# Performance work log

Hardware: AMD Instinct MI355X
Metric: run time of the kernel (lower is better)

The kernel has to match this reference:

```python
import jax, jax.numpy as jnp
import numpy as np

# ---- module hyperparameters (match init_kwargs) ----
SPATIAL = (32, 64)          # token grid, N = 32*64 = 2048
D_MODEL = 1024
N_HEADS = 16
HEAD_DIM = D_MODEL // N_HEADS  # 64
THETA = 10000.0
XPOS_SCALE_BASE = SPATIAL[0] * 2  # 64


def _rope_tables():
    """ND rotary (xpos) tables, lucidrains-style.
    Each spatial axis gets head_dim//ndim rotary channels; frequencies are
    interleave-repeated (r=2) to pair with rotate_half. Returns cos, sin,
    xpos scale, each [N, HEAD_DIM] float32."""
    nd = len(SPATIAL)
    dpa = HEAD_DIM // nd  # dims per axis (32)
    freqs_axes, scale_axes = [], []
    for size in SPATIAL:
        inv_freq = 1.0 / (THETA ** (np.arange(0, dpa, 2, dtype=np.float64) / dpa))
        t = np.arange(size, dtype=np.float64)
        f = np.repeat(t[:, None] * inv_freq[None, :], 2, axis=-1)        # [size, dpa]
        sbase = (np.arange(0, dpa, 2, dtype=np.float64) + 0.4 * dpa) / (1.4 * dpa)
        power = (t - size // 2) / XPOS_SCALE_BASE
        sc = np.repeat(sbase[None, :] ** power[:, None], 2, axis=-1)     # [size, dpa]
        freqs_axes.append(f)
        scale_axes.append(sc)
    # broadcast each axis table over the full grid, concat along channel dim
    def grid_concat(tabs):
        parts = []
        for i, tab in enumerate(tabs):
            shp = [1] * nd + [dpa]
            shp[i] = SPATIAL[i]
            parts.append(np.broadcast_to(tab.reshape(shp), tuple(SPATIAL) + (dpa,)))
        return np.concatenate(parts, axis=-1).reshape(-1, HEAD_DIM)  # [N, HEAD_DIM]
    freqs = grid_concat(freqs_axes)
    xscale = grid_concat(scale_axes)
    return (jnp.asarray(np.cos(freqs), jnp.float32),
            jnp.asarray(np.sin(freqs), jnp.float32),
            jnp.asarray(xscale, jnp.float32))


def _rotate_half(x):
    # pairwise rotation: (x1, x2) -> (-x2, x1), interleaved layout
    x = x.reshape(*x.shape[:-1], -1, 2)
    x1, x2 = x[..., 0], x[..., 1]
    return jnp.stack((-x2, x1), axis=-1).reshape(*x.shape[:-2], -1)


def setup_inputs() -> dict:
    key = jax.random.key(0)
    ks = jax.random.split(key, 3)
    B, N = 2, SPATIAL[0] * SPATIAL[1]
    x = jax.random.normal(ks[0], (B, N, D_MODEL), dtype=jnp.float32)
    w_qkv = jax.random.normal(ks[1], (D_MODEL, 3 * D_MODEL), dtype=jnp.float32) * 0.02
    b_qkv = jnp.zeros((3 * D_MODEL,), jnp.float32)
    w_proj = jax.random.normal(ks[2], (D_MODEL, D_MODEL), dtype=jnp.float32) * 0.02
    b_proj = jnp.zeros((D_MODEL,), jnp.float32)
    return {"x": x, "w_qkv": w_qkv, "b_qkv": b_qkv, "w_proj": w_proj, "b_proj": b_proj}


def reference(x, w_qkv, b_qkv, w_proj, b_proj):
    B, N, C = x.shape
    scale = HEAD_DIM ** -0.5
    qkv = (x @ w_qkv + b_qkv).reshape(B, N, 3, N_HEADS, HEAD_DIM)
    qkv = qkv.transpose(2, 0, 3, 1, 4)  # [3, B, H, N, D]
    q, k, v = qkv[0], qkv[1], qkv[2]
    cos, sin, xs = _rope_tables()       # [N, D], broadcast over B,H
    q = (q * cos + _rotate_half(q) * sin) * xs
    k = (k * cos + _rotate_half(k) * sin) / xs
    attn = jax.nn.softmax(jnp.einsum('bhnd,bhmd->bhnm', q, k) * scale, axis=-1)
    out = jnp.einsum('bhnm,bhmd->bhnd', attn, v)
    out = out.transpose(0, 2, 1, 3).reshape(B, N, C)
    return out @ w_proj + b_proj
```

## Files before the change

### kernel.cpp

```cpp
#include <hip/hip_runtime.h>
#include <math.h>

typedef __attribute__((ext_vector_type(8))) _Float16 f16x8;
typedef __attribute__((ext_vector_type(4))) _Float16 f16x4;
typedef __attribute__((ext_vector_type(4))) float f32x4;
typedef __attribute__((ext_vector_type(16))) float f32x16;

#define MFMAH(a, b, c) __builtin_amdgcn_mfma_f32_16x16x32_f16((a), (b), (c), 0, 0, 0)
#define MFMA32(a, b, c) __builtin_amdgcn_mfma_f32_32x32x16_f16((a), (b), (c), 0, 0, 0)

#define QSCALE 0.18033688011112042f
#define SOFF 4.328085122666891f


__device__ __forceinline__ void gl_lds16(const _Float16* g, _Float16* l) {
    __builtin_amdgcn_global_load_lds(
        (const __attribute__((address_space(1))) unsigned int*)g,
        (__attribute__((address_space(3))) unsigned int*)l, 16, 0, 0);
}

__device__ __forceinline__ unsigned pkh(float a, float b) {
    union { _Float16 h[2]; unsigned u; } x;
    x.h[0] = (_Float16)a;
    x.h[1] = (_Float16)b;
    return x.u;
}

__global__ void prep_kernel(const float* __restrict__ x, const float* __restrict__ w_qkv,
                            const float* __restrict__ w_proj, _Float16* __restrict__ xb,
                            _Float16* __restrict__ wq, _Float16* __restrict__ wp,
                            float* __restrict__ ct, float* __restrict__ st,
                            float* __restrict__ xt) {
    __shared__ float tile[32][33];
    const int b = blockIdx.x, tid = threadIdx.x;
    if (b < 4096) {
        int i = (b * 256 + tid) * 4;
        float4 v = *(const float4*)&x[i];
        f16x4 h = {(_Float16)v.x, (_Float16)v.y, (_Float16)v.z, (_Float16)v.w};
        *(f16x4*)&xb[i] = h;
    } else if (b < 4096 + 3072 + 1024) {
        int t, C;
        const float* src;
        _Float16* dst;
        if (b < 4096 + 3072) { t = b - 4096; C = 3072; src = w_qkv; dst = wq; }
        else                 { t = b - 4096 - 3072; C = 1024; src = w_proj; dst = wp; }
        const int tr = t & 31, tc = t >> 5;
        const int tx = tid & 31, ty = tid >> 5;
#pragma unroll
        for (int yy = 0; yy < 4; ++yy) {
            int r = ty + yy * 8;
            tile[r][tx] = src[(size_t)(tr * 32 + r) * C + tc * 32 + tx];
        }
        __syncthreads();
#pragma unroll
        for (int yy = 0; yy < 4; ++yy) {
            int r = ty + yy * 8;
            dst[(size_t)(tc * 32 + r) * 1024 + tr * 32 + tx] = (_Float16)tile[tx][r];
        }
    } else {
        int i = (b - 8192) * 256 + tid;
        int n = i >> 6, d = i & 63;
        int gi = n >> 6, gj = n & 63;
        int axis = d >> 5;
        int p = (d & 31) >> 1;
        float t = axis ? (float)gj : (float)gi;
        float half = axis ? 32.0f : 16.0f;
        float inv_freq = powf(10000.0f, -(float)p * (1.0f / 16.0f));
        float fr = t * inv_freq;
        float sbase = (2.0f * p + 12.8f) / 44.8f;
        float xs = powf(sbase, (t - half) * (1.0f / 64.0f));
        ct[i] = cosf(fr);
        st[i] = sinf(fr);
        xt[i] = xs;
    }
}

__global__ __launch_bounds__(256) void gemm_qkv_kernel(
    const _Float16* __restrict__ A_g, const _Float16* __restrict__ B_g,
    const float* __restrict__ bias, const float* __restrict__ ctab,
    const float* __restrict__ stab, const float* __restrict__ xtab,
    _Float16* __restrict__ qb, _Float16* __restrict__ kb, _Float16* __restrict__ vt) {
    __shared__ __align__(16) _Float16 Asm[4096];
    __shared__ __align__(16) _Float16 Bsm[4096];

    const int tid = threadIdx.x;
    const int lane = tid & 63, wave = tid >> 6;
    const int quad = lane >> 4, l16 = lane & 15;
    const int wm = wave >> 1, wn = wave & 1;
    const int m0 = blockIdx.x * 128, n0 = blockIdx.y * 128;

    f32x4 zero = {0.f, 0.f, 0.f, 0.f};
    f32x4 acc[4][4];
#pragma unroll
    for (int i = 0; i < 4; ++i)
#pragma unroll
        for (int j = 0; j < 4; ++j) acc[i][j] = zero;

    const int c1t = tid + 256;
    const int row0 = tid >> 2, s0 = tid & 3;
    const int row1 = c1t >> 2, s1 = c1t & 3;
    const int g0 = s0 ^ ((row0 >> 1) & 3);
    const int g1 = s1 ^ ((row1 >> 1) & 3);
    const _Float16* Ap0 = &A_g[(size_t)(m0 + row0) * 1024 + (g0 << 3)];
    const _Float16* Ap1 = &A_g[(size_t)(m0 + row1) * 1024 + (g1 << 3)];
    const _Float16* Bp0 = &B_g[(size_t)(n0 + row0) * 1024 + (g0 << 3)];
    const _Float16* Bp1 = &B_g[(size_t)(n0 + row1) * 1024 + (g1 << 3)];
    _Float16* La0 = &Asm[tid * 8];
    _Float16* La1 = &Asm[c1t * 8];
    _Float16* Lb0 = &Bsm[tid * 8];
    _Float16* Lb1 = &Bsm[c1t * 8];

    const int sw = (l16 >> 1) & 3;

    for (int k0 = 0; k0 < 1024; k0 += 32) {
        __syncthreads();
        gl_lds16(Ap0 + k0, La0);
        gl_lds16(Ap1 + k0, La1);
        gl_lds16(Bp0 + k0, Lb0);
        gl_lds16(Bp1 + k0, Lb1);
        __syncthreads();

        f16x8 af[4], bf[4];
#pragma unroll
        for (int i = 0; i < 4; ++i) {
            af[i] = *(const f16x8*)&Asm[(wm * 64 + i * 16 + l16) * 32 + ((quad ^ sw) << 3)];
            bf[i] = *(const f16x8*)&Bsm[(wn * 64 + i * 16 + l16) * 32 + ((quad ^ sw) << 3)];
        }
#pragma unroll
        for (int i = 0; i < 4; ++i)
#pragma unroll
            for (int j = 0; j < 4; ++j) acc[i][j] = MFMAH(af[i], bf[j], acc[i][j]);
    }

    float bj[4];
#pragma unroll
    for (int j = 0; j < 4; ++j) bj[j] = bias[n0 + wn * 64 + j * 16 + l16];

    if (n0 < 2048) {
#pragma unroll
        for (int i = 0; i < 4; ++i) {
#pragma unroll
            for (int r = 0; r < 4; ++r) {
                const int row = m0 + wm * 64 + i * 16 + quad * 4 + r;
                const int b = row >> 11, nrow = row & 2047;
#pragma unroll
                for (int j = 0; j < 4; ++j) {
                    const int col = n0 + wn * 64 + j * 16 + l16;
                    float v = acc[i][j][r] + bj[j];
                    float partner = __shfl_xor(v, 1);
                    const int hh = (col >> 6) & 15;
                    const int d = col & 63;
                    const size_t o = ((size_t)(b * 16 + hh) * 2048 + nrow) * 64 + d;
                    float rh = (d & 1) ? partner : -partner;
                    const int ti = nrow * 64 + d;
                    float rv = v * ctab[ti] + rh * stab[ti];
                    float xs = xtab[ti];
                    if (col < 1024)
                        qb[o] = (_Float16)(rv * xs * QSCALE);
                    else
                        kb[o] = (_Float16)(rv / xs);
                }
            }
        }
    } else {
#pragma unroll
        for (int i = 0; i < 4; ++i) {
            const int row = m0 + wm * 64 + i * 16 + quad * 4;
            const int b = row >> 11, nrow = row & 2047;
            const int nrp = (nrow & ~12) | ((nrow & 4) << 1) | ((nrow & 8) >> 1);
#pragma unroll
            for (int j = 0; j < 4; ++j) {
                const int col = n0 + wn * 64 + j * 16 + l16;
                const int hh = (col >> 6) & 15;
                const int d = col & 63;
                f16x4 pv4;
#pragma unroll
                for (int r = 0; r < 4; ++r) pv4[r] = (_Float16)(acc[i][j][r] + bj[j]);
                *(f16x4*)&vt[((size_t)(b * 16 + hh) * 64 + d) * 2048 + nrp] = pv4;
            }
        }
    }
}

__global__ __launch_bounds__(256) void gemm_proj_kernel(
    const _Float16* __restrict__ A_g, const _Float16* __restrict__ B_g,
    const float* __restrict__ bias, float* __restrict__ out) {
    __shared__ __align__(16) _Float16 Asm[4096];
    __shared__ __align__(16) _Float16 Bsm[4096];

    const int tid = threadIdx.x;
    const int lane = tid & 63, wave = tid >> 6;
    const int quad = lane >> 4, l16 = lane & 15;
    const int wm = wave >> 1, wn = wave & 1;
    const int m0 = blockIdx.x * 128, n0 = blockIdx.y * 128;

    f32x4 zero = {0.f, 0.f, 0.f, 0.f};
    f32x4 acc[4][4];
#pragma unroll
    for (int i = 0; i < 4; ++i)
#pragma unroll
        for (int j = 0; j < 4; ++j) acc[i][j] = zero;

    const int c1t = tid + 256;
    const int row0 = tid >> 2, s0 = tid & 3;
    const int row1 = c1t >> 2, s1 = c1t & 3;
    const int g0 = s0 ^ ((row0 >> 1) & 3);
    const int g1 = s1 ^ ((row1 >> 1) & 3);
    const _Float16* Ap0 = &A_g[(size_t)(m0 + row0) * 1024 + (g0 << 3)];
    const _Float16* Ap1 = &A_g[(size_t)(m0 + row1) * 1024 + (g1 << 3)];
    const _Float16* Bp0 = &B_g[(size_t)(n0 + row0) * 1024 + (g0 << 3)];
    const _Float16* Bp1 = &B_g[(size_t)(n0 + row1) * 1024 + (g1 << 3)];
    _Float16* La0 = &Asm[tid * 8];
    _Float16* La1 = &Asm[c1t * 8];
    _Float16* Lb0 = &Bsm[tid * 8];
    _Float16* Lb1 = &Bsm[c1t * 8];

    const int sw = (l16 >> 1) & 3;

    for (int k0 = 0; k0 < 1024; k0 += 32) {
        __syncthreads();
        gl_lds16(Ap0 + k0, La0);
        gl_lds16(Ap1 + k0, La1);
        gl_lds16(Bp0 + k0, Lb0);
        gl_lds16(Bp1 + k0, Lb1);
        __syncthreads();

        f16x8 af[4], bf[4];
#pragma unroll
        for (int i = 0; i < 4; ++i) {
            af[i] = *(const f16x8*)&Asm[(wm * 64 + i * 16 + l16) * 32 + ((quad ^ sw) << 3)];
            bf[i] = *(const f16x8*)&Bsm[(wn * 64 + i * 16 + l16) * 32 + ((quad ^ sw) << 3)];
        }
#pragma unroll
        for (int i = 0; i < 4; ++i)
#pragma unroll
            for (int j = 0; j < 4; ++j) acc[i][j] = MFMAH(af[i], bf[j], acc[i][j]);
    }

    float bj[4];
#pragma unroll
    for (int j = 0; j < 4; ++j) bj[j] = bias[n0 + wn * 64 + j * 16 + l16];
#pragma unroll
    for (int i = 0; i < 4; ++i)
#pragma unroll
        for (int r = 0; r < 4; ++r) {
            const int row = m0 + wm * 64 + i * 16 + quad * 4 + r;
#pragma unroll
            for (int j = 0; j < 4; ++j) {
                const int col = n0 + wn * 64 + j * 16 + l16;
                out[(size_t)row * 1024 + col] = acc[i][j][r] + bj[j];
            }
        }
}

#define KLD 72

__global__ __launch_bounds__(512) void attn_kernel(
    const _Float16* __restrict__ qb, const _Float16* __restrict__ kb,
    const _Float16* __restrict__ vt, _Float16* __restrict__ ao) {
    __shared__ __align__(16) _Float16 smem[8 * 64 * KLD];

    const int tid = threadIdx.x;
    const int lane = tid & 63, wave = tid >> 6;
    const int w4 = wave & 3, wgrp = wave >> 2;
    const int l32 = lane & 31, hi = lane >> 5, hi8 = hi << 3;
    const int bh = blockIdx.x & 31, qt = blockIdx.x >> 5;
    const size_t base = (size_t)bh * 2048 * 64;
    const int qrow0 = qt * 128 + w4 * 32;
    const int kbase = wgrp << 10;

    _Float16* K0 = &smem[(wgrp * 2 + 0) * 64 * KLD];
    _Float16* K1 = &smem[(wgrp * 2 + 1) * 64 * KLD];
    _Float16* V0 = &smem[(4 + wgrp * 2 + 0) * 64 * KLD];
    _Float16* V1 = &smem[(4 + wgrp * 2 + 1) * 64 * KLD];

    f16x8 qf[4];
#pragma unroll
    for (int dc = 0; dc < 4; ++dc)
        qf[dc] = *(const f16x8*)&qb[base + (size_t)(qrow0 + l32) * 64 + dc * 16 + hi8];

    f32x16 moff16, zero16;
#pragma unroll
    for (int e = 0; e < 16; ++e) { moff16[e] = -SOFF; zero16[e] = 0.f; }
    f32x16 o0 = zero16, o1 = zero16;
    float lsum = 0.f;

    const int t256 = tid & 255;
    const int kr0 = t256 >> 3, ko0 = (t256 & 7) << 3;
    const int kr1 = kr0 + 32;
    f16x8 pk0, pk1, pv0, pv1;
    auto gload = [&](int kt) {
        pk0 = *(const f16x8*)&kb[base + (size_t)(kt + kr0) * 64 + ko0];
        pk1 = *(const f16x8*)&kb[base + (size_t)(kt + kr1) * 64 + ko0];
        pv0 = *(const f16x8*)&vt[((size_t)bh * 64 + kr0) * 2048 + kt + ko0];
        pv1 = *(const f16x8*)&vt[((size_t)bh * 64 + kr1) * 2048 + kt + ko0];
    };
    auto stage = [&](_Float16* Ks, _Float16* Vs) {
        *(f16x8*)&Ks[kr0 * KLD + ko0] = pk0;
        *(f16x8*)&Ks[kr1 * KLD + ko0] = pk1;
        *(f16x8*)&Vs[kr0 * KLD + ko0] = pv0;
        *(f16x8*)&Vs[kr1 * KLD + ko0] = pv1;
    };

    auto compute = [&](const _Float16* Ks, const _Float16* Vs) {
        f32x16 s0 = moff16, s1 = moff16;
        __builtin_amdgcn_s_setprio(1);
#pragma unroll
        for (int dc = 0; dc < 4; ++dc) {
            f16x8 kf0 = *(const f16x8*)&Ks[l32 * KLD + dc * 16 + hi8];
            f16x8 kf1 = *(const f16x8*)&Ks[(32 + l32) * KLD + dc * 16 + hi8];
            s0 = MFMA32(kf0, qf[dc], s0);
            s1 = MFMA32(kf1, qf[dc], s1);
        }
        __builtin_amdgcn_s_setprio(0);
        float p0[16], p1[16];
#pragma unroll
        for (int e = 0; e < 16; ++e) {
            p0[e] = __builtin_amdgcn_exp2f(s0[e]);
            lsum += p0[e];
        }
#pragma unroll
        for (int e = 0; e < 16; ++e) {
            p1[e] = __builtin_amdgcn_exp2f(s1[e]);
            lsum += p1[e];
        }
        __builtin_amdgcn_s_setprio(1);
#pragma unroll
        for (int c = 0; c < 4; ++c) {
            const float* ps = (c < 2) ? p0 : p1;
            const int bo = (c & 1) * 8;
            union { unsigned w[4]; f16x8 v; } pf;
            pf.w[0] = pkh(ps[bo + 0], ps[bo + 1]);
            pf.w[1] = pkh(ps[bo + 2], ps[bo + 3]);
            pf.w[2] = pkh(ps[bo + 4], ps[bo + 5]);
            pf.w[3] = pkh(ps[bo + 6], ps[bo + 7]);
            f16x8 vf0 = *(const f16x8*)&Vs[l32 * KLD + c * 16 + hi8];
            f16x8 vf1 = *(const f16x8*)&Vs[(32 + l32) * KLD + c * 16 + hi8];
            o0 = MFMA32(pf.v, vf0, o0);
            o1 = MFMA32(pf.v, vf1, o1);
        }
        __builtin_amdgcn_s_setprio(0);
    };

    gload(kbase);
    stage(K0, V0);
    gload(kbase + 64);
    __syncthreads();

    for (int it = 0; it < 16; it += 2) {
        stage(K1, V1);
        if (it + 2 < 16) gload(kbase + (it + 2) * 64);
        compute(K0, V0);
        __syncthreads();
        if (it + 2 < 16) stage(K0, V0);
        if (it + 3 < 16) gload(kbase + (it + 3) * 64);
        compute(K1, V1);
        __syncthreads();
    }

    float vsum = lsum + __shfl_xor(lsum, 32);

    float* cb = (float*)smem;
    if (wgrp == 1) {
        float* p = &cb[(w4 * 64 + lane) * 33];
#pragma unroll
        for (int r = 0; r < 16; ++r) { p[r] = o0[r]; p[16 + r] = o1[r]; }
        p[32] = vsum;
    }
    __syncthreads();
    if (wgrp == 0) {
        const float* p = &cb[(w4 * 64 + lane) * 33];
#pragma unroll
        for (int r = 0; r < 16; ++r) { o0[r] += p[r]; o1[r] += p[16 + r]; }
        vsum += p[32];

        float vinv = 1.0f / vsum;
        float linv[16];
#pragma unroll
        for (int r = 0; r < 16; ++r)
            linv[r] = __shfl(vinv, (r & 3) + 8 * (r >> 2) + 4 * hi);

        const int b = bh >> 4, hh = bh & 15;
#pragma unroll
        for (int r = 0; r < 16; ++r) {
            const int qrow = qrow0 + (r & 3) + 8 * (r >> 2) + 4 * hi;
            const size_t oi = ((size_t)(b * 2048 + qrow)) * 1024 + hh * 64 + l32;
            ao[oi] = (_Float16)(o0[r] * linv[r]);
            ao[oi + 32] = (_Float16)(o1[r] * linv[r]);
        }
    }
}

extern "C" void kernel_launch(void* const* d_in, const int* in_sizes, int n_in,
                              void* d_out, int out_size, void* d_ws, size_t ws_size,
                              hipStream_t stream) {
    const float* x = (const float*)d_in[0];
    const float* w_qkv = (const float*)d_in[1];
    const float* b_qkv = (const float*)d_in[2];
    const float* w_proj = (const float*)d_in[3];
    const float* b_proj = (const float*)d_in[4];
    float* out = (float*)d_out;

    char* ws = (char*)d_ws;
    size_t off = 0;
    auto take = [&](size_t bytes) { char* p = ws + off; off += bytes; return p; };
    _Float16* xbuf   = (_Float16*)take(8388608);
    _Float16* wqkvT  = (_Float16*)take(6291456);
    _Float16* wprojT = (_Float16*)take(2097152);
    _Float16* qbuf   = (_Float16*)take(8388608);
    _Float16* kbuf   = (_Float16*)take(8388608);
    _Float16* vtbuf  = (_Float16*)take(8388608);
    float* ctab      = (float*)take(524288);
    float* stab      = (float*)take(524288);
    float* xtab      = (float*)take(524288);
    _Float16* ao = xbuf;

    prep_kernel<<<8704, 256, 0, stream>>>(x, w_qkv, w_proj, xbuf, wqkvT, wprojT,
                                          ctab, stab, xtab);
    gemm_qkv_kernel<<<dim3(32, 24), 256, 0, stream>>>(xbuf, wqkvT, b_qkv,
                                                      ctab, stab, xtab, qbuf, kbuf, vtbuf);
    attn_kernel<<<512, 512, 0, stream>>>(qbuf, kbuf, vtbuf, ao);
    gemm_proj_kernel<<<dim3(32, 8), 256, 0, stream>>>(ao, wprojT, b_proj, out);
}
```

Measured before the change: 196.6 us.

## Double-buffer LDS tiles in QKV and projection GEMMs to overlap loads

Both GEMM kernels now keep two shared-memory buffers per operand. Each iteration issues the direct global-to-LDS loads for the next K tile before running the MFMAs on the current one, and synchronises once per iteration instead of twice. The aim is to hide global memory latency behind compute and to cut barrier stalls. In exchange, LDS usage per block doubles, which can reduce occupancy, and correctness depends on the barrier waiting for the async LDS loads.

```diff
diff --git a/kernel.cpp b/kernel.cpp
--- a/kernel.cpp
+++ b/kernel.cpp
@@ -80,8 +80,8 @@
     const float* __restrict__ bias, const float* __restrict__ ctab,
     const float* __restrict__ stab, const float* __restrict__ xtab,
     _Float16* __restrict__ qb, _Float16* __restrict__ kb, _Float16* __restrict__ vt) {
-    __shared__ __align__(16) _Float16 Asm[4096];
-    __shared__ __align__(16) _Float16 Bsm[4096];
+    __shared__ __align__(16) _Float16 Asm[2][4096];
+    __shared__ __align__(16) _Float16 Bsm[2][4096];
 
     const int tid = threadIdx.x;
     const int lane = tid & 63, wave = tid >> 6;
@@ -105,31 +105,35 @@
     const _Float16* Ap1 = &A_g[(size_t)(m0 + row1) * 1024 + (g1 << 3)];
     const _Float16* Bp0 = &B_g[(size_t)(n0 + row0) * 1024 + (g0 << 3)];
     const _Float16* Bp1 = &B_g[(size_t)(n0 + row1) * 1024 + (g1 << 3)];
-    _Float16* La0 = &Asm[tid * 8];
-    _Float16* La1 = &Asm[c1t * 8];
-    _Float16* Lb0 = &Bsm[tid * 8];
-    _Float16* Lb1 = &Bsm[c1t * 8];
+
+    auto stage = [&](int buf, int k0) {
+        gl_lds16(Ap0 + k0, &Asm[buf][tid * 8]);
+        gl_lds16(Ap1 + k0, &Asm[buf][c1t * 8]);
+        gl_lds16(Bp0 + k0, &Bsm[buf][tid * 8]);
+        gl_lds16(Bp1 + k0, &Bsm[buf][c1t * 8]);
+    };
 
     const int sw = (l16 >> 1) & 3;
 
-    for (int k0 = 0; k0 < 1024; k0 += 32) {
+    stage(0, 0);
+    __syncthreads();
+
+    for (int t = 0; t < 32; ++t) {
+        const int cur = t & 1;
+        if (t + 1 < 32) stage(cur ^ 1, (t + 1) * 32);
+
+        f16x8 af[4], bf[4];
+#pragma unroll
+        for (int i = 0; i < 4; ++i) {
+            af[i] = *(const f16x8*)&Asm[cur][(wm * 64 + i * 16 + l16) * 32 + ((quad ^ sw) << 3)];
+            bf[i] = *(const f16x8*)&Bsm[cur][(wn * 64 + i * 16 + l16) * 32 + ((quad ^ sw) << 3)];
+        }
+#pragma unroll
+        for (int i = 0; i < 4; ++i)
+#pragma unroll
+            for (int j = 0; j < 4; ++j) acc[i][j] = MFMAH(af[i], bf[j], acc[i][j]);
+
         __syncthreads();
-        gl_lds16(Ap0 + k0, La0);
-        gl_lds16(Ap1 + k0, La1);
-        gl_lds16(Bp0 + k0, Lb0);
-        gl_lds16(Bp1 + k0, Lb1);
-        __syncthreads();
-
-        f16x8 af[4], bf[4];
-#pragma unroll
-        for (int i = 0; i < 4; ++i) {
-            af[i] = *(const f16x8*)&Asm[(wm * 64 + i * 16 + l16) * 32 + ((quad ^ sw) << 3)];
-            bf[i] = *(const f16x8*)&Bsm[(wn * 64 + i * 16 + l16) * 32 + ((quad ^ sw) << 3)];
-        }
-#pragma unroll
-        for (int i = 0; i < 4; ++i)
-#pragma unroll
-            for (int j = 0; j < 4; ++j) acc[i][j] = MFMAH(af[i], bf[j], acc[i][j]);
     }
 
     float bj[4];
@@ -185,8 +189,8 @@
 __global__ __launch_bounds__(256) void gemm_proj_kernel(
     const _Float16* __restrict__ A_g, const _Float16* __restrict__ B_g,
     const float* __restrict__ bias, float* __restrict__ out) {
-    __shared__ __align__(16) _Float16 Asm[4096];
-    __shared__ __align__(16) _Float16 Bsm[4096];
+    __shared__ __align__(16) _Float16 Asm[2][4096];
+    __shared__ __align__(16) _Float16 Bsm[2][4096];
 
     const int tid = threadIdx.x;
     const int lane = tid & 63, wave = tid >> 6;
@@ -210,31 +214,35 @@
     const _Float16* Ap1 = &A_g[(size_t)(m0 + row1) * 1024 + (g1 << 3)];
     const _Float16* Bp0 = &B_g[(size_t)(n0 + row0) * 1024 + (g0 << 3)];
     const _Float16* Bp1 = &B_g[(size_t)(n0 + row1) * 1024 + (g1 << 3)];
-    _Float16* La0 = &Asm[tid * 8];
-    _Float16* La1 = &Asm[c1t * 8];
-    _Float16* Lb0 = &Bsm[tid * 8];
-    _Float16* Lb1 = &Bsm[c1t * 8];
+
+    auto stage = [&](int buf, int k0) {
+        gl_lds16(Ap0 + k0, &Asm[buf][tid * 8]);
+        gl_lds16(Ap1 + k0, &Asm[buf][c1t * 8]);
+        gl_lds16(Bp0 + k0, &Bsm[buf][tid * 8]);
+        gl_lds16(Bp1 + k0, &Bsm[buf][c1t * 8]);
+    };
 
     const int sw = (l16 >> 1) & 3;
 
-    for (int k0 = 0; k0 < 1024; k0 += 32) {
+    stage(0, 0);
+    __syncthreads();
+
+    for (int t = 0; t < 32; ++t) {
+        const int cur = t & 1;
+        if (t + 1 < 32) stage(cur ^ 1, (t + 1) * 32);
+
+        f16x8 af[4], bf[4];
+#pragma unroll
+        for (int i = 0; i < 4; ++i) {
+            af[i] = *(const f16x8*)&Asm[cur][(wm * 64 + i * 16 + l16) * 32 + ((quad ^ sw) << 3)];
+            bf[i] = *(const f16x8*)&Bsm[cur][(wn * 64 + i * 16 + l16) * 32 + ((quad ^ sw) << 3)];
+        }
+#pragma unroll
+        for (int i = 0; i < 4; ++i)
+#pragma unroll
+            for (int j = 0; j < 4; ++j) acc[i][j] = MFMAH(af[i], bf[j], acc[i][j]);
+
         __syncthreads();
-        gl_lds16(Ap0 + k0, La0);
-        gl_lds16(Ap1 + k0, La1);
-        gl_lds16(Bp0 + k0, Lb0);
-        gl_lds16(Bp1 + k0, Lb1);
-        __syncthreads();
-
-        f16x8 af[4], bf[4];
-#pragma unroll
-        for (int i = 0; i < 4; ++i) {
-            af[i] = *(const f16x8*)&Asm[(wm * 64 + i * 16 + l16) * 32 + ((quad ^ sw) << 3)];
-            bf[i] = *(const f16x8*)&Bsm[(wn * 64 + i * 16 + l16) * 32 + ((quad ^ sw) << 3)];
-        }
-#pragma unroll
-        for (int i = 0; i < 4; ++i)
-#pragma unroll
-            for (int j = 0; j < 4; ++j) acc[i][j] = MFMAH(af[i], bf[j], acc[i][j]);
     }
 
     float bj[4];
```

New measurement: 203.4 us. 3.4% more time.
